# Kernel tuning notes

Measured on AMD Instinct MI355X. Metric: run time of the kernel, lower is better.

The kernel has to match this reference:

```python
import jax, jax.numpy as jnp
import numpy as np


def complex_relu(v):
    # mask by sign of real part, applied to the full complex value
    return (v.real >= 0) * v


def magnetic_laplacian(senders, receivers, n_node, n_nodes, q=0.25):
    """Symmetric-normalized magnetic Laplacian, [b, n, n] complex64.

    Faithful to the source with default q_absolute=0.25 (truthy), so the
    `else` branch (constant q per graph) is taken.
    """
    b = senders.shape[0]
    edges_padding_mask = (senders >= 0).astype(jnp.float32)  # [b, e]
    # adj[b, s, r] += mask[s]  (faithful scatter, incl. the d[s] gather)
    def assign(a, s, r, d):
        return a.at[s, r].add(d[s])
    adj = jax.vmap(assign)(
        jnp.zeros((b, n_nodes, n_nodes), jnp.float32),
        senders, receivers, edges_padding_mask)
    adj = jnp.where(adj > 1, 1.0, adj)
    adj_t = jnp.swapaxes(adj, -1, -2)
    sym_adj = adj + adj_t
    sym_adj = jnp.where((adj != 0) & (adj_t != 0), sym_adj / 2, sym_adj)
    sym_deg = sym_adj.sum(-2)  # [b, n]
    qv = jnp.full(b, q, dtype=jnp.float32)  # q_absolute branch
    theta = 1j * 2 * jnp.pi * qv[:, None, None] * (adj - adj_t)
    # diagonal D^{-1/2}; diag-matmul expressed as row/col scaling (same math)
    inv_sqrt_deg = jax.lax.rsqrt(jnp.clip(sym_deg, 1))  # [b, n]
    norm_adj = inv_sqrt_deg[:, :, None] * sym_adj * inv_sqrt_deg[:, None, :]
    laplacian = jnp.eye(n_nodes) - norm_adj * jnp.exp(theta)
    idx = jnp.arange(n_nodes)[None, :]  # [1, n]
    node_mask = idx < n_node[:, :1]  # [b, n]
    pair_mask = node_mask[:, :, None] * node_mask[:, None, :]  # [b, n, n]
    return pair_mask * laplacian


def _magnet_forward(nodes, senders, receivers, n_node,
                    w0_0, b0_0, w1_0, w0_1, b0_1, w1_1):
    b, n, d = nodes.shape
    lap = magnetic_laplacian(senders, receivers, n_node, n)
    max_eigenvalue = jnp.linalg.eigvalsh(lap).max()  # scalar over batch
    eye = jnp.eye(n, dtype=lap.dtype)
    t_1 = (2.0 / max_eigenvalue) * lap - eye[None]  # [b, n, n] complex
    x = nodes + 0j  # complex64 state
    for w0, b0, w1 in ((w0_0, b0_0, w1_0), (w0_1, b0_1, w1_1)):
        # t_0 = I, so t_0 @ x == x
        x_0 = (x.real @ w0 + b0) + 1j * (x.imag @ w0 + b0)
        x_t1 = t_1 @ x  # [b, n, d] complex
        x_1 = (x_t1.real @ w1) + 1j * (x_t1.imag @ w1)
        x = complex_relu(x_0 + x_1)
    return jnp.concatenate((x.real, x.imag), axis=-1)  # [b, n, 2*d_model]


def setup_inputs() -> dict:
    key = jax.random.key(0)
    ks = jax.random.split(key, 10)
    b, n, e, d = 64, 512, 4096, 256
    scale = 1.0 / np.sqrt(d)
    return {
        "nodes": jax.random.normal(ks[0], (b, n, d), jnp.float32),
        "senders": jax.random.randint(ks[1], (b, e), 0, n, dtype=jnp.int32),
        "receivers": jax.random.randint(ks[2], (b, e), 0, n, dtype=jnp.int32),
        "n_node": jax.random.randint(ks[3], (b, 1), 0, n, dtype=jnp.int32),
        "w0_0": jax.random.normal(ks[4], (d, d), jnp.float32) * scale,
        "b0_0": jnp.zeros((d,), jnp.float32),
        "w1_0": jax.random.normal(ks[5], (d, d), jnp.float32) * scale,
        "w0_1": jax.random.normal(ks[6], (d, d), jnp.float32) * scale,
        "b0_1": jnp.zeros((d,), jnp.float32),
        "w1_1": jax.random.normal(ks[7], (d, d), jnp.float32) * scale,
    }


def reference(nodes, senders, receivers, n_node,
              w0_0, b0_0, w1_0, w0_1, b0_1, w1_1):
    return _magnet_forward(nodes, senders, receivers, n_node,
                           w0_0, b0_0, w1_0, w0_1, b0_1, w1_1)
```

## Files before the change

kernel.cpp:

```cpp
#include <hip/hip_runtime.h>
#include <stdint.h>

typedef unsigned long long u64;
typedef unsigned int u32;
typedef unsigned short u16;

#define BATCH 64
#define NN    512
#define NAUG  1024
#define DM    256
#define NEDGE 4096
#define CAP   64
#define PK2   32
#define PK2A  36
#define LM    128

#define OFF_ADJ   ((size_t)0)
#define SZ_ADJ    ((size_t)BATCH*NN*8*8)
#define OFF_ADJT  (OFF_ADJ + SZ_ADJ)
#define OFF_LAM   (OFF_ADJT + SZ_ADJ)
#define OFF_LMX   (OFF_LAM + 64)
#define OFF_PK2   (OFF_LAM + 1024)
#define SZ_PK2    ((size_t)BATCH*PK2A*NN*16)
#define OFF_DEGI  (OFF_PK2 + SZ_PK2)
#define OFF_LENS  (OFF_DEGI + (size_t)BATCH*NN*4)
#define OFF_ENTS  (OFF_LENS + (size_t)BATCH*NN*4)
#define OFF_VALS  (OFF_ENTS + (size_t)BATCH*NN*CAP*4)
#define OFF_XF    (OFF_VALS + (size_t)BATCH*NN*CAP*4)
#define OFF_XT1   (OFF_XF  + (size_t)BATCH*NAUG*DM*4)
#define OFF_S     (OFF_XT1 + (size_t)BATCH*NAUG*DM*4)

__global__ void k_scatter(const int* __restrict__ senders, const int* __restrict__ receivers,
                          u64* __restrict__ adj, u64* __restrict__ adjT){
    int idx = blockIdx.x * 256 + threadIdx.x;
    int b = idx >> 12;
    int s = senders[idx];
    int r = receivers[idx];
    if (s >= 0){
        atomicOr(&adj [((size_t)b*NN + s)*8 + (r >> 6)], 1ull << (r & 63));
        atomicOr(&adjT[((size_t)b*NN + r)*8 + (s >> 6)], 1ull << (s & 63));
    }
}

__global__ void k_deg(const u64* __restrict__ adj, const u64* __restrict__ adjT,
                      float* __restrict__ degInv){
    int idx = blockIdx.x * 256 + threadIdx.x;
    const u64* a = adj  + (size_t)idx * 8;
    const u64* t = adjT + (size_t)idx * 8;
    int deg = 0;
#pragma unroll
    for (int w = 0; w < 8; ++w) deg += __popcll(a[w] | t[w]);
    degInv[idx] = (float)(1.0 / sqrt((double)(deg < 1 ? 1 : deg)));
}

__global__ __launch_bounds__(256)
void k_build(const u64* __restrict__ adj, const u64* __restrict__ adjT,
             const float* __restrict__ degInv, const int* __restrict__ n_node,
             u32* __restrict__ ents, float* __restrict__ vals, int* __restrict__ lens,
             uint2* __restrict__ pk2, int* __restrict__ lmax){
    int gw   = (blockIdx.x * 256 + threadIdx.x) >> 6;
    int lane = threadIdx.x & 63;
    int b = gw >> 9;
    int i = gw & (NN - 1);
    const u64* arow = adj  + ((size_t)b*NN + i)*8;
    const u64* trow = adjT + ((size_t)b*NN + i)*8;
    int wsel = lane >> 3, sh = (lane & 7) * 8;
    u32 ba = (u32)((arow[wsel] >> sh) & 0xFFull);
    u32 bt = (u32)((trow[wsel] >> sh) & 0xFFull);
    int nn_b = n_node[b];
    bool mi  = i < nn_b;
    float di = degInv[b*NN + i];
    int j0 = lane * 8;

    float vr_[8], vi_[8];
    int cnt = 0;
#pragma unroll
    for (int jj = 0; jj < 8; ++jj){
        int j = j0 + jj;
        int a = (ba >> jj) & 1, t = (bt >> jj) & 1;
        bool mm = mi && (j < nn_b);
        float c = di * degInv[b*NN + j];
        float vr = 0.f, vi = 0.f;
        if (j == i){
            if (mm) vr = 1.0f - (a ? c : 0.0f);
        } else if (mm && ((a | t) != 0)){
            if (a & t)      vr = -c;
            else if (a)     vi = -c;
            else            vi =  c;
        }
        vr_[jj] = vr; vi_[jj] = vi;
        cnt += (vr != 0.f || vi != 0.f) ? 1 : 0;
    }
    int off = cnt;
#pragma unroll
    for (int d = 1; d < 64; d <<= 1){
        int nb = __shfl_up(off, d);
        if (lane >= d) off += nb;
    }
    int excl = off - cnt;
    int tot  = __shfl(off, 63);
    int p = excl;
    u32*   erow = ents + ((size_t)b*NN + i)*CAP;
    float* vrow = vals + ((size_t)b*NN + i)*CAP;
#pragma unroll
    for (int jj = 0; jj < 8; ++jj){
        float vr = vr_[jj], vi = vi_[jj];
        if (vr != 0.f || vi != 0.f){
            if (p < CAP){
                int ty = (vi != 0.f) ? 1 : 0;
                int j = j0 + jj;
                float v = ty ? vi : vr;
                erow[p] = (u32)j | ((u32)ty << 9);
                vrow[p] = v;
                size_t slot = ((size_t)b*PK2A + (p >> 1))*NN + i;
                pk2[slot*2 + (p & 1)] =
                    make_uint2((u32)((j << 3) + (ty << 12)), __float_as_uint(v));
            }
            p++;
        }
    }
    if (lane == 63){
        int tc = tot > CAP ? CAP : tot;
        lens[b*NN + i] = tc;
        atomicMax(&lmax[b], tc);
    }
}

#define DO_G4(S0)                                                         \
    {                                                                     \
        float2 vva = VALS[S0][tid];                                       \
        float2 vvb = VALS[S0+1][tid];                                     \
        u32 opa = offp[S0], opb = offp[S0+1];                             \
        float2 u0 = *(const float2*)((const char*)XY + (opa & 0xFFFFu));  \
        float2 u1 = *(const float2*)((const char*)XY + (opa >> 16));      \
        float2 u2 = *(const float2*)((const char*)XY + (opb & 0xFFFFu));  \
        float2 u3 = *(const float2*)((const char*)XY + (opb >> 16));      \
        wr0 = fmaf(vva.x, u0.x, wr0); wi0 = fmaf(vva.x, u0.y, wi0);       \
        wr0 = fmaf(vva.y, u1.x, wr0); wi0 = fmaf(vva.y, u1.y, wi0);       \
        wr1 = fmaf(vvb.x, u2.x, wr1); wi1 = fmaf(vvb.x, u2.y, wi1);       \
        wr1 = fmaf(vvb.y, u3.x, wr1); wi1 = fmaf(vvb.y, u3.y, wi1);       \
        float2 vvc = VALS[S0+2][tid];                                     \
        float2 vvd = VALS[S0+3][tid];                                     \
        u32 opc = offp[S0+2], opd = offp[S0+3];                           \
        float2 u4 = *(const float2*)((const char*)XY + (opc & 0xFFFFu));  \
        float2 u5 = *(const float2*)((const char*)XY + (opc >> 16));      \
        float2 u6 = *(const float2*)((const char*)XY + (opd & 0xFFFFu));  \
        float2 u7 = *(const float2*)((const char*)XY + (opd >> 16));      \
        wr0 = fmaf(vvc.x, u4.x, wr0); wi0 = fmaf(vvc.x, u4.y, wi0);       \
        wr0 = fmaf(vvc.y, u5.x, wr0); wi0 = fmaf(vvc.y, u5.y, wi0);       \
        wr1 = fmaf(vvd.x, u6.x, wr1); wi1 = fmaf(vvd.x, u6.y, wi1);       \
        wr1 = fmaf(vvd.y, u7.x, wr1); wi1 = fmaf(vvd.y, u7.y, wi1);       \
    }

__global__ __launch_bounds__(512)
void k_lanczos(const uint4* __restrict__ pk2, const int* __restrict__ lens,
               float* __restrict__ lam){
    int b = blockIdx.x;
    int tid = threadIdx.x;
    int w = tid >> 6, l = tid & 63;
    __shared__ float2 XY[2*NN];
    __shared__ float2 VALS[PK2][NN];
    __shared__ float alphS[LM], betS[LM];
    __shared__ float redA[8], redB[8];
    __shared__ int bCnt[PK2 + 1], bOff[PK2 + 1];
    __shared__ u16 sortRow[NN];
    const uint4* base = pk2 + (size_t)b*PK2A*NN;

    if (tid <= PK2) bCnt[tid] = 0;
    __syncthreads();
    int defES = (lens[b*NN + tid] + 1) >> 1;
    atomicAdd(&bCnt[defES], 1);
    __syncthreads();
    if (tid == 0){
        int acc = 0;
        for (int e = PK2; e >= 0; --e){ bOff[e] = acc; acc += bCnt[e]; }
    }
    __syncthreads();
    int pos = atomicAdd(&bOff[defES], 1);
    sortRow[pos] = (u16)tid;
    __syncthreads();
    int row  = sortRow[tid];
    int myES = (lens[b*NN + row] + 1) >> 1;

    u32 offp[PK2];
#pragma unroll
    for (int s = 0; s < PK2; ++s){
        uint4 q = base[(size_t)s*NN + row];
        offp[s] = (q.x & 0xFFFFu) | (q.z << 16);
        VALS[s][tid] = make_float2(__uint_as_float(q.y), __uint_as_float(q.w));
    }

    u32 h = (u32)row * 2654435761u + 0x9E3779B9u;
    h ^= h >> 16; h *= 0x85EBCA6Bu; h ^= h >> 13;
    float xr = (float)(h & 0xFFFF) * (1.f/65536.f) - 0.5f;
    h = h * 1664525u + 1013904223u;
    float xi = (float)(h & 0xFFFF) * (1.f/65536.f) - 0.5f;
    float ss = xr*xr + xi*xi;
#pragma unroll
    for (int d = 1; d < 64; d <<= 1) ss += __shfl_xor(ss, d);
    if (l == 0) redA[w] = ss;
    __syncthreads();
    float inv0 = 1.f / sqrtf(redA[0] + redA[1] + redA[2] + redA[3]
                           + redA[4] + redA[5] + redA[6] + redA[7]);
    xr *= inv0; xi *= inv0;
    XY[row]      = make_float2(xr, xi);
    XY[NN + row] = make_float2(-xi, xr);
    __syncthreads();
    float v0r = 0.f, v0i = 0.f;
    float betaPrev = 0.f;
    int mEff = LM;
    for (int j = 0; j < LM; ++j){
        float wr0 = 0.f, wi0 = 0.f, wr1 = 0.f, wi1 = 0.f;
        if (myES >  0) DO_G4(0);
        if (myES >  4) DO_G4(4);
        if (myES >  8) DO_G4(8);
        if (myES > 12) DO_G4(12);
        if (myES > 16) DO_G4(16);
        if (myES > 20) DO_G4(20);
        if (myES > 24) DO_G4(24);
        if (myES > 28) DO_G4(28);
        float wr = wr0 + wr1, wi = wi0 + wi1;
        float pa = xr*wr + xi*wi;
#pragma unroll
        for (int d = 1; d < 64; d <<= 1) pa += __shfl_xor(pa, d);
        if (l == 0) redA[w] = pa;
        __syncthreads();
        float paF = redA[0] + redA[1] + redA[2] + redA[3]
                  + redA[4] + redA[5] + redA[6] + redA[7];
        wr -= paF*xr + betaPrev*v0r;
        wi -= paF*xi + betaPrev*v0i;
        float pb = wr*wr + wi*wi;
#pragma unroll
        for (int d = 1; d < 64; d <<= 1) pb += __shfl_xor(pb, d);
        if (l == 0) redB[w] = pb;
        __syncthreads();
        float pbF = redB[0] + redB[1] + redB[2] + redB[3]
                  + redB[4] + redB[5] + redB[6] + redB[7];
        float bta = sqrtf(pbF);
        if (w == 0 && l == 0){ alphS[j] = paF; betS[j] = bta; }
        if (pbF < 1e-14f){ mEff = j + 1; break; }
        float binv = 1.f / bta;
        float nr = wr * binv;
        float ni = wi * binv;
        v0r = xr; v0i = xi;
        xr = nr; xi = ni;
        XY[row]      = make_float2(nr, ni);
        XY[NN + row] = make_float2(-ni, nr);
        __syncthreads();
        betaPrev = bta;
    }
    if (w == 0){
        int m = mEff;
        double lo = -0.5, hi = 2.5;
        for (int sweep = 0; sweep < 5; ++sweep){
            double wd = (hi - lo) * (1.0/65.0);
            double mid = lo + wd * (double)(l + 1);
            int cnt = 0;
            double d = (double)alphS[0] - mid;
            if (d < 0.0) cnt++;
            for (int k = 1; k < m; ++k){
                if (d == 0.0) d = -1e-300;
                double bk = (double)betS[k-1];
                d = ((double)alphS[k] - mid) - bk*bk/d;
                if (d < 0.0) cnt++;
            }
            u64 mask = __ballot(cnt >= m);
            if (mask == 0ull){
                lo = lo + wd * 64.0;
            } else {
                int L = __ffsll(mask) - 1;
                hi = lo + wd * (double)(L + 1);
                lo = lo + wd * (double)L;
            }
        }
        if (l == 0){
            float l1 = (float)hi;
            if (l1 < 0.f) l1 = 0.f;
            if (l1 > 2.0f) l1 = 2.0f;
            atomicMax((u32*)lam, __float_as_uint(l1));
        }
    }
}

__global__ void k_prep32(const float* __restrict__ nodes, float* __restrict__ xf){
    int row = blockIdx.x;
    int t = threadIdx.x;
    int b = row >> 10, i = row & (NAUG - 1);
    float v = (i < NN) ? nodes[((size_t)b*NN + i)*DM + t] : 0.f;
    xf[(size_t)row*DM + t] = v;
}

__global__ __launch_bounds__(256)
void k_spmm(const u32* __restrict__ ents, const float* __restrict__ vals,
            const int* __restrict__ lens, const float* __restrict__ xf,
            const float* __restrict__ lam, float* __restrict__ xt1){
    int i = blockIdx.x;
    int b = blockIdx.y;
    int t = threadIdx.x;
    int len = lens[b*NN + i];
    const u32*   er = ents + ((size_t)b*NN + i)*CAP;
    const float* ev = vals + ((size_t)b*NN + i)*CAP;
    const float* xb = xf + (size_t)b*NAUG*DM;
    double ar = 0.0, ai = 0.0;
    for (int e = 0; e < len; ++e){
        u32 en = er[e];
        double v = (double)ev[e];
        int j = en & 511;
        double xr = (double)xb[(size_t)j*DM + t];
        double xi = (double)xb[(size_t)(NN + j)*DM + t];
        if (en & 512u){ ar = fma(v, -xi, ar); ai = fma(v, xr, ai); }
        else          { ar = fma(v,  xr, ar); ai = fma(v, xi, ai); }
    }
    double alpha = 2.0 / (double)lam[0];
    size_t ro = ((size_t)b*NAUG + i)*DM + t;
    size_t io = ((size_t)b*NAUG + NN + i)*DM + t;
    xt1[ro] = (float)(alpha*ar - (double)xf[ro]);
    xt1[io] = (float)(alpha*ai - (double)xf[io]);
}

__global__ __launch_bounds__(256)
void k_gemm32(const float* __restrict__ xf, const float* __restrict__ xt1,
              const float* __restrict__ w0, const float* __restrict__ w1,
              const float* __restrict__ bias, float* __restrict__ sOut){
    __shared__ float As[32][68];
    __shared__ float Bs[32][68];
    int m0 = blockIdx.y * 64;
    int n0 = blockIdx.x * 64;
    int tid = threadIdx.x;
    int tx = tid & 15, ty = tid >> 4;
    double acc[4][4];
#pragma unroll
    for (int r = 0; r < 4; ++r)
#pragma unroll
        for (int c = 0; c < 4; ++c) acc[r][c] = 0.0;
    for (int ph = 0; ph < 2; ++ph){
        const float* A = ph ? xt1 : xf;
        const float* W = ph ? w1 : w0;
        for (int k0 = 0; k0 < DM; k0 += 32){
#pragma unroll
            for (int l = 0; l < 2; ++l){
                int fi = tid + l*256;
                int m  = fi >> 3, c4 = fi & 7;
                float4 g = *(const float4*)(A + ((size_t)(m0 + m))*DM + k0 + c4*4);
                As[c4*4+0][m] = g.x; As[c4*4+1][m] = g.y;
                As[c4*4+2][m] = g.z; As[c4*4+3][m] = g.w;
                int kk = fi >> 4, n4 = fi & 15;
                float4 hh = *(const float4*)(W + ((size_t)(k0 + kk))*DM + n0 + n4*4);
                *(float4*)&Bs[kk][n4*4] = hh;
            }
            __syncthreads();
            float facc[4][4];
#pragma unroll
            for (int r = 0; r < 4; ++r)
#pragma unroll
                for (int c = 0; c < 4; ++c) facc[r][c] = 0.f;
#pragma unroll
            for (int kk = 0; kk < 32; ++kk){
                float4 a4 = *(const float4*)&As[kk][ty*4];
                float4 b4 = *(const float4*)&Bs[kk][tx*4];
                facc[0][0] = fmaf(a4.x, b4.x, facc[0][0]);
                facc[0][1] = fmaf(a4.x, b4.y, facc[0][1]);
                facc[0][2] = fmaf(a4.x, b4.z, facc[0][2]);
                facc[0][3] = fmaf(a4.x, b4.w, facc[0][3]);
                facc[1][0] = fmaf(a4.y, b4.x, facc[1][0]);
                facc[1][1] = fmaf(a4.y, b4.y, facc[1][1]);
                facc[1][2] = fmaf(a4.y, b4.z, facc[1][2]);
                facc[1][3] = fmaf(a4.y, b4.w, facc[1][3]);
                facc[2][0] = fmaf(a4.z, b4.x, facc[2][0]);
                facc[2][1] = fmaf(a4.z, b4.y, facc[2][1]);
                facc[2][2] = fmaf(a4.z, b4.z, facc[2][2]);
                facc[2][3] = fmaf(a4.z, b4.w, facc[2][3]);
                facc[3][0] = fmaf(a4.w, b4.x, facc[3][0]);
                facc[3][1] = fmaf(a4.w, b4.y, facc[3][1]);
                facc[3][2] = fmaf(a4.w, b4.z, facc[3][2]);
                facc[3][3] = fmaf(a4.w, b4.w, facc[3][3]);
            }
#pragma unroll
            for (int r = 0; r < 4; ++r)
#pragma unroll
                for (int c = 0; c < 4; ++c) acc[r][c] += (double)facc[r][c];
            __syncthreads();
        }
    }
    float4 bi = *(const float4*)(bias + n0 + tx*4);
#pragma unroll
    for (int r = 0; r < 4; ++r){
        float4 o;
        o.x = (float)(acc[r][0] + (double)bi.x);
        o.y = (float)(acc[r][1] + (double)bi.y);
        o.z = (float)(acc[r][2] + (double)bi.z);
        o.w = (float)(acc[r][3] + (double)bi.w);
        *(float4*)&sOut[((size_t)(m0 + ty*4 + r))*DM + n0 + tx*4] = o;
    }
}

__global__ void k_combine32(const float* __restrict__ sIn, float* __restrict__ xf,
                            float* __restrict__ out, int isFinal){
    int i = blockIdx.x;
    int b = blockIdx.y;
    int t = threadIdx.x;
    size_t ro = ((size_t)b*NAUG + i)*DM + t;
    size_t io = ((size_t)b*NAUG + NN + i)*DM + t;
    float re = sIn[ro], im = sIn[io];
    if (!(re >= 0.f)){ re = 0.f; im = 0.f; }
    if (isFinal){
        out[((size_t)b*NN + i)*(2*DM) + t]      = re;
        out[((size_t)b*NN + i)*(2*DM) + DM + t] = im;
    } else {
        xf[ro] = re; xf[io] = im;
    }
}

extern "C" void kernel_launch(void* const* d_in, const int* in_sizes, int n_in,
                              void* d_out, int out_size, void* d_ws, size_t ws_size,
                              hipStream_t stream){
    const float* nodes   = (const float*)d_in[0];
    const int*   senders = (const int*)  d_in[1];
    const int*   recvs   = (const int*)  d_in[2];
    const int*   n_node  = (const int*)  d_in[3];
    const float* w00     = (const float*)d_in[4];
    const float* b00     = (const float*)d_in[5];
    const float* w10     = (const float*)d_in[6];
    const float* w01     = (const float*)d_in[7];
    const float* b01     = (const float*)d_in[8];
    const float* w11     = (const float*)d_in[9];
    char* ws = (char*)d_ws;
    u64*   adj    = (u64*)  (ws + OFF_ADJ);
    u64*   adjT   = (u64*)  (ws + OFF_ADJT);
    float* lam    = (float*)(ws + OFF_LAM);
    int*   lmax   = (int*)  (ws + OFF_LMX);
    uint2* pk2    = (uint2*)(ws + OFF_PK2);
    float* degInv = (float*)(ws + OFF_DEGI);
    int*   lens   = (int*)  (ws + OFF_LENS);
    u32*   ents   = (u32*)  (ws + OFF_ENTS);
    float* vals   = (float*)(ws + OFF_VALS);
    float* xf     = (float*)(ws + OFF_XF);
    float* xt1    = (float*)(ws + OFF_XT1);
    float* sBuf   = (float*)(ws + OFF_S);
    float* out    = (float*)d_out;

    hipMemsetAsync(ws + OFF_ADJ, 0, OFF_PK2 + SZ_PK2, stream);

    k_scatter<<<dim3(BATCH*NEDGE/256), dim3(256), 0, stream>>>(senders, recvs, adj, adjT);
    k_deg    <<<dim3(BATCH*NN/256),    dim3(256), 0, stream>>>(adj, adjT, degInv);
    k_build  <<<dim3(BATCH*NN/4),      dim3(256), 0, stream>>>(adj, adjT, degInv, n_node,
                                                               ents, vals, lens, pk2, lmax);
    k_lanczos<<<dim3(BATCH),           dim3(512), 0, stream>>>((const uint4*)pk2, lens, lam);
    k_prep32 <<<dim3(BATCH*NAUG),      dim3(256), 0, stream>>>(nodes, xf);

    for (int layer = 0; layer < 2; ++layer){
        const float* w0 = layer ? w01 : w00;
        const float* w1 = layer ? w11 : w10;
        const float* bias = layer ? b01 : b00;
        k_spmm   <<<dim3(NN, BATCH),   dim3(256), 0, stream>>>(ents, vals, lens, xf, lam, xt1);
        k_gemm32 <<<dim3(DM/64, BATCH*NAUG/64), dim3(256), 0, stream>>>(xf, xt1, w0, w1, bias, sBuf);
        k_combine32<<<dim3(NN, BATCH), dim3(256), 0, stream>>>(sBuf, xf, out, layer);
    }
}
```

Baseline: 1.172 ms.

## Fuse complex ReLU into GEMM epilogue and skip zero imaginary rows in layer 0

The GEMM tile now interleaves the real and imaginary rows of the same nodes, so each thread holds both parts and can apply the complex ReLU mask in its epilogue. This removes the separate combine kernel and its round trip of the intermediate buffer. In layer 0 the input's imaginary part is zero, so those A rows are neither loaded nor multiplied in the x@w0 phase. Layer outputs are written to a second buffer or straight to the final output, and the layer loop is unrolled into explicit launches.

After: 1.325 ms. 1.13x slower.

```diff
diff --git a/kernel.cpp b/kernel.cpp
--- a/kernel.cpp
+++ b/kernel.cpp
@@ -319,31 +319,38 @@
 }
 
 __global__ __launch_bounds__(256)
-void k_gemm32(const float* __restrict__ xf, const float* __restrict__ xt1,
+void k_gemm32(const float* __restrict__ A0, const float* __restrict__ xt1,
               const float* __restrict__ w0, const float* __restrict__ w1,
-              const float* __restrict__ bias, float* __restrict__ sOut){
+              const float* __restrict__ bias, float* __restrict__ dst, int layer){
     __shared__ float As[32][68];
     __shared__ float Bs[32][68];
-    int m0 = blockIdx.y * 64;
+    int by = blockIdx.y;
+    int b  = by >> 4;
+    int i0 = (by & 15) * 32;
     int n0 = blockIdx.x * 64;
     int tid = threadIdx.x;
     int tx = tid & 15, ty = tid >> 4;
+    size_t abase = (size_t)b*NAUG*DM;
     double acc[4][4];
 #pragma unroll
     for (int r = 0; r < 4; ++r)
 #pragma unroll
         for (int c = 0; c < 4; ++c) acc[r][c] = 0.0;
     for (int ph = 0; ph < 2; ++ph){
-        const float* A = ph ? xt1 : xf;
+        const float* A = ph ? xt1 : A0;
         const float* W = ph ? w1 : w0;
+        int skipOdd = (layer == 0) && (ph == 0);
         for (int k0 = 0; k0 < DM; k0 += 32){
 #pragma unroll
             for (int l = 0; l < 2; ++l){
                 int fi = tid + l*256;
                 int m  = fi >> 3, c4 = fi & 7;
-                float4 g = *(const float4*)(A + ((size_t)(m0 + m))*DM + k0 + c4*4);
-                As[c4*4+0][m] = g.x; As[c4*4+1][m] = g.y;
-                As[c4*4+2][m] = g.z; As[c4*4+3][m] = g.w;
+                if (!(skipOdd && (m & 1))){
+                    size_t grow = abase + (size_t)((m & 1)*NN + i0 + (m >> 1))*DM;
+                    float4 g = *(const float4*)(A + grow + k0 + c4*4);
+                    As[c4*4+0][m] = g.x; As[c4*4+1][m] = g.y;
+                    As[c4*4+2][m] = g.z; As[c4*4+3][m] = g.w;
+                }
                 int kk = fi >> 4, n4 = fi & 15;
                 float4 hh = *(const float4*)(W + ((size_t)(k0 + kk))*DM + n0 + n4*4);
                 *(float4*)&Bs[kk][n4*4] = hh;
@@ -354,26 +361,42 @@
             for (int r = 0; r < 4; ++r)
 #pragma unroll
                 for (int c = 0; c < 4; ++c) facc[r][c] = 0.f;
-#pragma unroll
-            for (int kk = 0; kk < 32; ++kk){
-                float4 a4 = *(const float4*)&As[kk][ty*4];
-                float4 b4 = *(const float4*)&Bs[kk][tx*4];
-                facc[0][0] = fmaf(a4.x, b4.x, facc[0][0]);
-                facc[0][1] = fmaf(a4.x, b4.y, facc[0][1]);
-                facc[0][2] = fmaf(a4.x, b4.z, facc[0][2]);
-                facc[0][3] = fmaf(a4.x, b4.w, facc[0][3]);
-                facc[1][0] = fmaf(a4.y, b4.x, facc[1][0]);
-                facc[1][1] = fmaf(a4.y, b4.y, facc[1][1]);
-                facc[1][2] = fmaf(a4.y, b4.z, facc[1][2]);
-                facc[1][3] = fmaf(a4.y, b4.w, facc[1][3]);
-                facc[2][0] = fmaf(a4.z, b4.x, facc[2][0]);
-                facc[2][1] = fmaf(a4.z, b4.y, facc[2][1]);
-                facc[2][2] = fmaf(a4.z, b4.z, facc[2][2]);
-                facc[2][3] = fmaf(a4.z, b4.w, facc[2][3]);
-                facc[3][0] = fmaf(a4.w, b4.x, facc[3][0]);
-                facc[3][1] = fmaf(a4.w, b4.y, facc[3][1]);
-                facc[3][2] = fmaf(a4.w, b4.z, facc[3][2]);
-                facc[3][3] = fmaf(a4.w, b4.w, facc[3][3]);
+            if (skipOdd){
+#pragma unroll
+                for (int kk = 0; kk < 32; ++kk){
+                    float4 a4 = *(const float4*)&As[kk][ty*4];
+                    float4 b4 = *(const float4*)&Bs[kk][tx*4];
+                    facc[0][0] = fmaf(a4.x, b4.x, facc[0][0]);
+                    facc[0][1] = fmaf(a4.x, b4.y, facc[0][1]);
+                    facc[0][2] = fmaf(a4.x, b4.z, facc[0][2]);
+                    facc[0][3] = fmaf(a4.x, b4.w, facc[0][3]);
+                    facc[2][0] = fmaf(a4.z, b4.x, facc[2][0]);
+                    facc[2][1] = fmaf(a4.z, b4.y, facc[2][1]);
+                    facc[2][2] = fmaf(a4.z, b4.z, facc[2][2]);
+                    facc[2][3] = fmaf(a4.z, b4.w, facc[2][3]);
+                }
+            } else {
+#pragma unroll
+                for (int kk = 0; kk < 32; ++kk){
+                    float4 a4 = *(const float4*)&As[kk][ty*4];
+                    float4 b4 = *(const float4*)&Bs[kk][tx*4];
+                    facc[0][0] = fmaf(a4.x, b4.x, facc[0][0]);
+                    facc[0][1] = fmaf(a4.x, b4.y, facc[0][1]);
+                    facc[0][2] = fmaf(a4.x, b4.z, facc[0][2]);
+                    facc[0][3] = fmaf(a4.x, b4.w, facc[0][3]);
+                    facc[1][0] = fmaf(a4.y, b4.x, facc[1][0]);
+                    facc[1][1] = fmaf(a4.y, b4.y, facc[1][1]);
+                    facc[1][2] = fmaf(a4.y, b4.z, facc[1][2]);
+                    facc[1][3] = fmaf(a4.y, b4.w, facc[1][3]);
+                    facc[2][0] = fmaf(a4.z, b4.x, facc[2][0]);
+                    facc[2][1] = fmaf(a4.z, b4.y, facc[2][1]);
+                    facc[2][2] = fmaf(a4.z, b4.z, facc[2][2]);
+                    facc[2][3] = fmaf(a4.z, b4.w, facc[2][3]);
+                    facc[3][0] = fmaf(a4.w, b4.x, facc[3][0]);
+                    facc[3][1] = fmaf(a4.w, b4.y, facc[3][1]);
+                    facc[3][2] = fmaf(a4.w, b4.z, facc[3][2]);
+                    facc[3][3] = fmaf(a4.w, b4.w, facc[3][3]);
+                }
             }
 #pragma unroll
             for (int r = 0; r < 4; ++r)
@@ -383,31 +406,30 @@
         }
     }
     float4 bi = *(const float4*)(bias + n0 + tx*4);
+    float4 o[4];
 #pragma unroll
     for (int r = 0; r < 4; ++r){
-        float4 o;
-        o.x = (float)(acc[r][0] + (double)bi.x);
-        o.y = (float)(acc[r][1] + (double)bi.y);
-        o.z = (float)(acc[r][2] + (double)bi.z);
-        o.w = (float)(acc[r][3] + (double)bi.w);
-        *(float4*)&sOut[((size_t)(m0 + ty*4 + r))*DM + n0 + tx*4] = o;
-    }
-}
-
-__global__ void k_combine32(const float* __restrict__ sIn, float* __restrict__ xf,
-                            float* __restrict__ out, int isFinal){
-    int i = blockIdx.x;
-    int b = blockIdx.y;
-    int t = threadIdx.x;
-    size_t ro = ((size_t)b*NAUG + i)*DM + t;
-    size_t io = ((size_t)b*NAUG + NN + i)*DM + t;
-    float re = sIn[ro], im = sIn[io];
-    if (!(re >= 0.f)){ re = 0.f; im = 0.f; }
-    if (isFinal){
-        out[((size_t)b*NN + i)*(2*DM) + t]      = re;
-        out[((size_t)b*NN + i)*(2*DM) + DM + t] = im;
-    } else {
-        xf[ro] = re; xf[io] = im;
+        o[r].x = (float)(acc[r][0] + (double)bi.x);
+        o[r].y = (float)(acc[r][1] + (double)bi.y);
+        o[r].z = (float)(acc[r][2] + (double)bi.z);
+        o[r].w = (float)(acc[r][3] + (double)bi.w);
+    }
+#pragma unroll
+    for (int q = 0; q < 2; ++q){
+        float4 re = o[q*2], im = o[q*2 + 1];
+        float4 gr, gi;
+        gr.x = (re.x >= 0.f) ? re.x : 0.f;  gi.x = (re.x >= 0.f) ? im.x : 0.f;
+        gr.y = (re.y >= 0.f) ? re.y : 0.f;  gi.y = (re.y >= 0.f) ? im.y : 0.f;
+        gr.z = (re.z >= 0.f) ? re.z : 0.f;  gi.z = (re.z >= 0.f) ? im.z : 0.f;
+        gr.w = (re.w >= 0.f) ? re.w : 0.f;  gi.w = (re.w >= 0.f) ? im.w : 0.f;
+        int i = i0 + ty*2 + q;
+        if (layer == 0){
+            *(float4*)&dst[((size_t)b*NAUG + i)*DM      + n0 + tx*4] = gr;
+            *(float4*)&dst[((size_t)b*NAUG + NN + i)*DM + n0 + tx*4] = gi;
+        } else {
+            *(float4*)&dst[((size_t)(b*NN + i))*(2*DM)      + n0 + tx*4] = gr;
+            *(float4*)&dst[((size_t)(b*NN + i))*(2*DM) + DM + n0 + tx*4] = gi;
+        }
     }
 }
 
@@ -436,7 +458,7 @@
     float* vals   = (float*)(ws + OFF_VALS);
     float* xf     = (float*)(ws + OFF_XF);
     float* xt1    = (float*)(ws + OFF_XT1);
-    float* sBuf   = (float*)(ws + OFF_S);
+    float* xf2    = (float*)(ws + OFF_S);
     float* out    = (float*)d_out;
 
     hipMemsetAsync(ws + OFF_ADJ, 0, OFF_PK2 + SZ_PK2, stream);
@@ -448,12 +470,8 @@
     k_lanczos<<<dim3(BATCH),           dim3(512), 0, stream>>>((const uint4*)pk2, lens, lam);
     k_prep32 <<<dim3(BATCH*NAUG),      dim3(256), 0, stream>>>(nodes, xf);
 
-    for (int layer = 0; layer < 2; ++layer){
-        const float* w0 = layer ? w01 : w00;
-        const float* w1 = layer ? w11 : w10;
-        const float* bias = layer ? b01 : b00;
-        k_spmm   <<<dim3(NN, BATCH),   dim3(256), 0, stream>>>(ents, vals, lens, xf, lam, xt1);
-        k_gemm32 <<<dim3(DM/64, BATCH*NAUG/64), dim3(256), 0, stream>>>(xf, xt1, w0, w1, bias, sBuf);
-        k_combine32<<<dim3(NN, BATCH), dim3(256), 0, stream>>>(sBuf, xf, out, layer);
-    }
-}
+    k_spmm  <<<dim3(NN, BATCH),        dim3(256), 0, stream>>>(ents, vals, lens, xf, lam, xt1);
+    k_gemm32<<<dim3(DM/64, BATCH*16),  dim3(256), 0, stream>>>(xf, xt1, w00, w10, b00, xf2, 0);
+    k_spmm  <<<dim3(NN, BATCH),        dim3(256), 0, stream>>>(ents, vals, lens, xf2, lam, xt1);
+    k_gemm32<<<dim3(DM/64, BATCH*16),  dim3(256), 0, stream>>>(xf2, xt1, w01, w11, b01, out, 1);
+}
```
